# Kernel optimization log

Measured on AMD Instinct MI355X. Metric: run time of the kernel, lower is better.

Reference implementation:

```python
import jax, jax.numpy as jnp
import numpy as np

D = 1024      # d_model
B = 8         # batch
S = 512       # seq
L = 2         # GRU layers
DEPTH = 3     # min_depth == max_depth -> fixed recursion depth
EPS_RMS = 1.1920929e-07  # torch fp32 finfo eps (nn.RMSNorm default)


def setup_inputs() -> dict:
    key = jax.random.key(0)
    ks = jax.random.split(key, 16)

    def glorot(k, shape):
        fan_out, fan_in = shape
        lim = float(np.sqrt(6.0 / (fan_in + fan_out)))
        return jax.random.uniform(k, shape, jnp.float32, -lim, lim)

    gs = float(1.0 / np.sqrt(D))  # torch GRU init: U(-1/sqrt(H), 1/sqrt(H))
    inp = {
        "x": jax.random.normal(ks[0], (B, S, D), jnp.float32),
        # reflect: Linear -> RMSNorm -> GELU -> Linear -> RMSNorm
        "w1": glorot(ks[1], (D, D)), "b1": jnp.zeros(D, jnp.float32),
        "rms1_w": jnp.ones(D, jnp.float32),
        "w2": glorot(ks[2], (D, D)), "b2": jnp.zeros(D, jnp.float32),
        "rms2_w": jnp.ones(D, jnp.float32),
        "residual_weight": jnp.float32(0.5),
        # IntegrationMeasure projections (xavier_uniform, zero bias)
        "whole_w": glorot(ks[3], (D // 2, D)), "whole_b": jnp.zeros(D // 2, jnp.float32),
        "parts_w": glorot(ks[4], (D // 2, D)), "parts_b": jnp.zeros(D // 2, jnp.float32),
        "phi_scale": jnp.float32(1.0), "phi_bias": jnp.float32(0.0),
    }
    ki = 5
    for l in range(L):
        inp[f"wih{l}"] = jax.random.uniform(ks[ki + 0], (3 * D, D), jnp.float32, -gs, gs)
        inp[f"whh{l}"] = jax.random.uniform(ks[ki + 1], (3 * D, D), jnp.float32, -gs, gs)
        inp[f"bih{l}"] = jax.random.uniform(ks[ki + 2], (3 * D,), jnp.float32, -gs, gs)
        inp[f"bhh{l}"] = jax.random.uniform(ks[ki + 3], (3 * D,), jnp.float32, -gs, gs)
        ki += 4
    return inp


def _rmsnorm(x, w):
    ms = jnp.mean(x * x, axis=-1, keepdims=True)
    return x * jax.lax.rsqrt(ms + EPS_RMS) * w


def _gru_layer(seq, h0, Wih, Whh, bih, bhh):
    """seq: [S,B,D], h0: [B,D] -> (outputs [S,B,D], h_final [B,D]). torch gate order r,z,n."""
    def step(h, xt):
        gi = xt @ Wih.T + bih                       # [B, 3D]
        gh = h @ Whh.T + bhh                        # [B, 3D]
        ir, iz, ig = jnp.split(gi, 3, axis=-1)
        hr, hz, hg = jnp.split(gh, 3, axis=-1)
        r = jax.nn.sigmoid(ir + hr)
        z = jax.nn.sigmoid(iz + hz)
        n = jnp.tanh(ig + r * hg)
        hn = (1.0 - z) * n + z * h
        return hn, hn
    hT, ys = jax.lax.scan(step, h0, seq)
    return ys, hT


def reference(x, w1, b1, rms1_w, w2, b2, rms2_w, residual_weight,
              wih0, whh0, bih0, bhh0, wih1, whh1, bih1, bhh1,
              whole_w, whole_b, parts_w, parts_b, phi_scale, phi_bias):
    gru = [(wih0, whh0, bih0, bhh0), (wih1, whh1, bih1, bhh1)]
    batch = x.shape[0]
    hidden = [jnp.zeros((batch, D), x.dtype) for _ in range(L)]
    history = []  # detached states
    phi = None

    for loop in range(DEPTH):
        # self-reflection block
        h = _rmsnorm(x @ w1.T + b1, rms1_w)
        h = jax.nn.gelu(h, approximate=False)
        h = _rmsnorm(h @ w2.T + b2, rms2_w)
        x_ref = x + residual_weight * (h - x)
        # GRU integration (seq-first)
        seq = jnp.transpose(x_ref, (1, 0, 2))       # [S,B,D]
        new_hidden = []
        for l in range(L):
            seq, hT = _gru_layer(seq, hidden[l], *gru[l])
            new_hidden.append(hT)
        hidden = new_hidden
        x = jnp.transpose(seq, (0, 1, 2)).transpose(1, 0, 2)  # [B,S,D]
        # Phi (IntegrationMeasure) -- manifold_norm == L2 norm, fully vectorized
        whole = x @ whole_w.T + whole_b             # [B,S,D/2]
        whole_info = jnp.linalg.norm(whole, axis=-1).mean(axis=-1)  # [B]
        if len(history) == 0:
            phi = jnp.broadcast_to(jax.nn.sigmoid(phi_bias) * 0.3, (batch,))
        else:
            parts = jnp.stack(history) @ parts_w.T + parts_b      # [H,B,S,D/2]
            parts_info = jnp.linalg.norm(parts, axis=-1).mean(axis=-1).mean(axis=0)  # [B]
            raw_phi = (whole_info - parts_info) / (whole_info + 1e-08)
            phi = jnp.clip(phi_scale * raw_phi + phi_bias, 0.0, 1.0)
        history.append(jax.lax.stop_gradient(x))    # torch: x.clone().detach()

    return x, phi
```

## Files before the change

### kernel.cpp

```cpp
#include <hip/hip_runtime.h>
#include <math.h>

#define Dm 1024
#define Bm 8
#define Sm 512

typedef short s16x8 __attribute__((ext_vector_type(8)));
typedef float f32x4 __attribute__((ext_vector_type(4)));
typedef unsigned short u16;
typedef unsigned long long u64;

__device__ __forceinline__ float bf2f(u16 u) {
  union { float f; unsigned v; } x; x.v = (unsigned)u << 16; return x.f;
}
__device__ __forceinline__ u16 f2bf(float f) {
  union { float f; unsigned v; } x; x.f = f;
  unsigned r = x.v + 0x7FFFu + ((x.v >> 16) & 1u);
  return (u16)(r >> 16);
}
__device__ __forceinline__ float sigm(float x) { return 1.f / (1.f + expf(-x)); }

__device__ __forceinline__ u64 cld64(const void* p) {
  return __hip_atomic_load((const u64*)p, __ATOMIC_RELAXED, __HIP_MEMORY_SCOPE_AGENT);
}
__device__ __forceinline__ float cldf(const void* p) {
  return __hip_atomic_load((const float*)p, __ATOMIC_RELAXED, __HIP_MEMORY_SCOPE_AGENT);
}
__device__ __forceinline__ void cx64(void* p, u64 v) {
  u64 old = __hip_atomic_exchange((u64*)p, v, __ATOMIC_RELAXED, __HIP_MEMORY_SCOPE_AGENT);
  asm volatile("" :: "v"(old));
}
__device__ __forceinline__ void cst32(void* p, unsigned v) {
  __hip_atomic_store((unsigned*)p, v, __ATOMIC_RELAXED, __HIP_MEMORY_SCOPE_AGENT);
}

__global__ void k_conv(const float* __restrict__ x, const float* __restrict__ w1,
                       const float* __restrict__ w2, const float* __restrict__ ww,
                       const float* __restrict__ pw,
                       u16* __restrict__ Xb, u16* __restrict__ Wc,
                       float* __restrict__ Hf, u16* __restrict__ Hb,
                       float* __restrict__ sums, unsigned* __restrict__ flags,
                       unsigned* __restrict__ poison)
{
  long gid = (long)blockIdx.x * blockDim.x + threadIdx.x;
  const long N0 = 4194304, N1 = 1048576, N2 = 1048576, N3 = 524288, N4 = 524288;
  const long T = N0 + N1 + N2 + N3 + N4;
  for (long p = gid; p < T; p += (long)gridDim.x * blockDim.x) {
    long q = p;
    if (q < N0) { Xb[q] = f2bf(x[q]); continue; }
    q -= N0;
    if (q < N1) { Wc[q] = f2bf(w1[q]); continue; }
    q -= N1;
    if (q < N2) { Wc[N1 + q] = f2bf(w2[q]); continue; }
    q -= N2;
    if (q < N3) { Wc[N1 + N2 + q] = f2bf(ww[q]); continue; }
    q -= N3;
    Wc[N1 + N2 + N3 + q] = f2bf(pw[q]);
  }
  if (gid < 65536) flags[gid] = 0;
  if (gid < 2 * Bm * Dm) Hf[gid] = 0.f;
  if (gid < 262144) Hb[gid] = 0;
  if (gid < 16) sums[gid] = 0.f;
  if (gid == 0) *poison = 0;
}

template<int MODE>
__global__ __launch_bounds__(512)
void k_gemm(const u16* __restrict__ A, const u16* __restrict__ W,
            const float* __restrict__ bias, const float* __restrict__ nw,
            const u16* __restrict__ XresB, const float* __restrict__ rwp,
            u16* __restrict__ out0, float* __restrict__ sumdst, int Ncols)
{
  __shared__ u16 At[16 * 1024];
  __shared__ float rowsq[16];
  const int tid = threadIdx.x;
  const int lane = tid & 63, wv = tid >> 6;
  const int rlo = lane & 15, khi = lane >> 4;
  const int m0 = blockIdx.x * 16;

  {
    int row = tid & 15, c = tid >> 4;
    const char* src = (const char*)(A + (long)(m0 + row) * Dm);
    char* dst = (char*)At + row * 2048;
    int sw = (row & 7) << 4;
#pragma unroll
    for (int i = 0; i < 4; ++i) {
      int bo = c * 64 + i * 16;
      s16x8 v = *(const s16x8*)(src + bo);
      *(s16x8*)(dst + (bo ^ sw)) = v;
    }
  }
  __syncthreads();

  const int j0 = wv * 128;
  const bool act = j0 < Ncols;
  f32x4 zero4 = {0.f, 0.f, 0.f, 0.f};
  f32x4 acc[8];
#pragma unroll
  for (int jt = 0; jt < 8; ++jt) acc[jt] = zero4;

  if (act) {
    const u16* wbase = W + (long)(j0 + rlo) * Dm + khi * 8;
    const char* abase = (const char*)At + rlo * 2048;
    const int asw = (rlo & 7) << 4;
#pragma unroll
    for (int ks = 0; ks < 32; ++ks) {
      s16x8 a = *(const s16x8*)(abase + (((ks * 32 + khi * 8) * 2) ^ asw));
#pragma unroll
      for (int jt = 0; jt < 8; ++jt) {
        s16x8 b = *(const s16x8*)(wbase + (long)jt * 16 * Dm + ks * 32);
        acc[jt] = __builtin_amdgcn_mfma_f32_16x16x32_bf16(a, b, acc[jt], 0, 0, 0);
      }
    }
  }

  if (tid < 16) rowsq[tid] = 0.f;
  __syncthreads();

  float vals[8][4];
  if (act) {
    float rs[4] = {0.f, 0.f, 0.f, 0.f};
#pragma unroll
    for (int jt = 0; jt < 8; ++jt) {
      float bj = bias[j0 + jt * 16 + rlo];
#pragma unroll
      for (int r = 0; r < 4; ++r) {
        float v = acc[jt][r] + bj;
        vals[jt][r] = v;
        rs[r] += v * v;
      }
    }
#pragma unroll
    for (int r = 0; r < 4; ++r) {
#pragma unroll
      for (int m = 1; m < 16; m <<= 1) rs[r] += __shfl_xor(rs[r], m, 64);
    }
    if (rlo == 0) {
#pragma unroll
      for (int r = 0; r < 4; ++r) atomicAdd(&rowsq[khi * 4 + r], rs[r]);
    }
  }
  __syncthreads();

  if constexpr (MODE == 2) {
    if (tid < 16) {
      int token = m0 + tid;
      atomicAdd(&sumdst[token >> 9], sqrtf(rowsq[tid]));
    }
    return;
  } else {
    float rw = 0.f;
    if constexpr (MODE == 1) rw = rwp[0];
    if (act) {
#pragma unroll
      for (int jt = 0; jt < 8; ++jt) {
        int col = j0 + jt * 16 + rlo;
        float nwv = nw[col];
#pragma unroll
        for (int r = 0; r < 4; ++r) {
          int row = khi * 4 + r;
          int token = m0 + row;
          float ms = rowsq[row] * (1.f / 1024.f) + 1.1920929e-07f;
          float y = vals[jt][r] * rsqrtf(ms) * nwv;
          if constexpr (MODE == 0) {
            y = 0.5f * y * (1.f + erff(y * 0.7071067811865476f));
            out0[(long)token * Dm + col] = f2bf(y);
          } else {
            float xf = bf2f(XresB[(long)token * Dm + col]);
            float xr = xf + rw * (y - xf);
            u16 hi = f2bf(xr);
            float lo = xr - bf2f(hi);
            int s = token & (Sm - 1), b = token >> 9;
            long base = ((long)s * 16 + b) * Dm + col;
            out0[base] = hi;
            out0[base + 8 * Dm] = f2bf(lo);
          }
        }
      }
    }
  }
}

#define SPIN_CAP 2000000

__device__ __forceinline__ bool spin2(const unsigned* pA, bool enA, const unsigned* pB,
                                      unsigned val, unsigned* poison) {
  int spins = 0;
  while (true) {
    bool c = !enA || (__hip_atomic_load(pA, __ATOMIC_RELAXED, __HIP_MEMORY_SCOPE_AGENT) >= val);
    if (pB) c = c && (__hip_atomic_load(pB, __ATOMIC_RELAXED, __HIP_MEMORY_SCOPE_AGENT) >= val);
    if (__all(c)) return true;
    __builtin_amdgcn_s_sleep(1);
    if ((++spins & 255) == 0) {
      if (__hip_atomic_load(poison, __ATOMIC_RELAXED, __HIP_MEMORY_SCOPE_AGENT)) return false;
      if (spins > SPIN_CAP) {
        __hip_atomic_store(poison, 1u, __ATOMIC_RELAXED, __HIP_MEMORY_SCOPE_AGENT);
        return false;
      }
    }
  }
}

__global__ __launch_bounds__(256, 1)
void k_rec(const float* __restrict__ wih0, const float* __restrict__ whh0,
           const float* __restrict__ bih0, const float* __restrict__ bhh0,
           const float* __restrict__ wih1, const float* __restrict__ whh1,
           const float* __restrict__ bih1, const float* __restrict__ bhh1,
           const u16* __restrict__ XrefB,
           float* __restrict__ gi0r, float* __restrict__ gi1r,
           u16* __restrict__ Hb, float* __restrict__ Hf,
           u16* __restrict__ Xb, float* __restrict__ outx,
           unsigned* __restrict__ flags, unsigned* __restrict__ poison, int loop)
{
  __shared__ float part[4][3][16][33];
  __shared__ unsigned pflag;

  const int wg = blockIdx.x;
  const int role = wg >> 5;
  const int w = wg & 31;
  const int d0 = w * 32;
  const int tid = threadIdx.x;
  const int lane = tid & 63, q = tid >> 6;
  const int rlo = lane & 15, khi = lane >> 4;
  const unsigned val = (unsigned)loop + 1u;

  unsigned* F0 = flags;
  unsigned* F1 = flags + 16384;
  unsigned* F2 = flags + 32768;
  unsigned* F3 = flags + 49152;
  u16* Hb0 = Hb;
  u16* Hb1 = Hb + 8 * 16384;

  if (tid == 0) pflag = 0;

  const float* Wsel = (role == 0) ? wih0 : (role == 1) ? whh0 : (role == 2) ? wih1 : whh1;

  s16x8 bfr[8][3][2];
#pragma unroll
  for (int ks = 0; ks < 8; ++ks)
#pragma unroll
    for (int g = 0; g < 3; ++g)
#pragma unroll
      for (int jt = 0; jt < 2; ++jt) {
        int rowj = g * 1024 + d0 + jt * 16 + rlo;
        const float* p = Wsel + (long)rowj * Dm + q * 256 + ks * 32 + khi * 8;
        s16x8 f;
#pragma unroll
        for (int e = 0; e < 8; ++e) f[e] = (short)f2bf(p[e]);
        bfr[ks][g][jt] = f;
      }

  const int ob = tid >> 5, odd = tid & 31, od = d0 + odd;
  float bias_r[3];
  {
    const float* bsel = (role == 0) ? bih0 : (role == 1) ? bhh0 : (role == 2) ? bih1 : bhh1;
#pragma unroll
    for (int g = 0; g < 3; ++g) bias_r[g] = bsel[g * 1024 + od];
  }
  const int layer = (role == 1) ? 0 : 1;
  float hreg = 0.f;
  if (role == 1 || role == 3) hreg = Hf[layer * 8192 + ob * 1024 + od];
  __syncthreads();

  for (int t = 0; t < Sm; ++t) {
    if (q == 0) {
      const unsigned* pA;
      const unsigned* pB = nullptr;
      bool enA;
      bool need = true;
      if (role == 0) {
        pA = &F1[((t >= 8) ? (t - 8) : 0) * 32 + w];
        enA = true;
        need = (t >= 8);
      } else if (role == 1) {
        pA = (lane < 32) ? &F1[((t >= 1) ? (t - 1) : 0) * 32 + lane]
                         : &F2[((t >= 8) ? (t - 8) : 0) * 32 + (lane - 32)];
        enA = (lane < 32) ? (t >= 1) : (t >= 8);
        pB = &F0[t * 32 + w];
      } else if (role == 2) {
        pA = (lane < 32) ? &F1[t * 32 + lane]
                         : &F3[((t >= 8) ? (t - 8) : 0) * 32 + (lane - 32)];
        enA = (lane < 32) ? true : (t >= 8);
      } else {
        pA = &F3[((t >= 1) ? (t - 1) : 0) * 32 + ((lane < 32) ? lane : (lane - 32))];
        enA = (lane < 32) && (t >= 1);
        pB = &F2[t * 32 + w];
      }
      if (need) {
        if (!spin2(pA, enA, pB, val, poison)) { if (lane == 0) pflag = 1; }
      }
    }
    __builtin_amdgcn_sched_barrier(0);
    __syncthreads();
    if (pflag) return;

    float giv[3] = {0.f, 0.f, 0.f};
    if (role == 1 || role == 3) {
      const float* ring = ((role == 1) ? gi0r : gi1r) + ((long)(t & 7) * Bm + ob) * 3072 + od;
      giv[0] = cldf(ring);
      giv[1] = cldf(ring + 1024);
      giv[2] = cldf(ring + 2048);
    }

    s16x8 areg[8];
    if (role == 0) {
      const u16* src = XrefB + (long)t * 16 * Dm + rlo * 1024 + q * 256 + khi * 8;
#pragma unroll
      for (int ks = 0; ks < 8; ++ks)
        areg[ks] = *(const s16x8*)(src + ks * 32);
    } else {
      const u16* base = (role == 1) ? Hb0 + ((t - 1) & 7) * 16384
                      : (role == 2) ? Hb0 + (t & 7) * 16384
                                    : Hb1 + ((t - 1) & 7) * 16384;
      const u16* src = base + rlo * 1024 + q * 256 + khi * 8;
#pragma unroll
      for (int ks = 0; ks < 8; ++ks) {
        union { u64 u[2]; s16x8 v; } tmp;
        tmp.u[0] = cld64(src + ks * 32);
        tmp.u[1] = cld64(src + ks * 32 + 4);
        areg[ks] = tmp.v;
      }
    }

    f32x4 zero4 = {0.f, 0.f, 0.f, 0.f};
    f32x4 acc[3][2];
#pragma unroll
    for (int g = 0; g < 3; ++g) { acc[g][0] = zero4; acc[g][1] = zero4; }
#pragma unroll
    for (int ks = 0; ks < 8; ++ks)
#pragma unroll
      for (int g = 0; g < 3; ++g)
#pragma unroll
        for (int jt = 0; jt < 2; ++jt)
          acc[g][jt] = __builtin_amdgcn_mfma_f32_16x16x32_bf16(areg[ks], bfr[ks][g][jt], acc[g][jt], 0, 0, 0);

#pragma unroll
    for (int g = 0; g < 3; ++g)
#pragma unroll
      for (int jt = 0; jt < 2; ++jt)
#pragma unroll
        for (int r = 0; r < 4; ++r)
          part[q][g][khi * 4 + r][jt * 16 + rlo] = acc[g][jt][r];
    __syncthreads();

    {
      int b = ob, dd = odd;
      float v[3];
#pragma unroll
      for (int g = 0; g < 3; ++g) {
        float sv = 0.f;
#pragma unroll
        for (int qq = 0; qq < 4; ++qq)
          sv += part[qq][g][b][dd] + part[qq][g][8 + b][dd];
        v[g] = sv;
      }
      if (role == 0 || role == 2) {
        float* ring = ((role == 0) ? gi0r : gi1r) + ((long)(t & 7) * Bm + b) * 3072 + od;
#pragma unroll
        for (int g = 0; g < 3; ++g) {
          float fg = v[g] + bias_r[g];
          float pg = __shfl_xor(fg, 1, 64);
          if ((dd & 1) == 0) {
            union { float f; unsigned u; } a0, a1;
            a0.f = fg; a1.f = pg;
            u64 pk = (u64)a0.u | ((u64)a1.u << 32);
            cx64(ring + g * 1024, pk);
          }
        }
      } else {
        float gr = giv[0] + v[0] + bias_r[0];
        float gz = giv[1] + v[1] + bias_r[1];
        float ghn = v[2] + bias_r[2];
        float rr = sigm(gr), zz = sigm(gz);
        float nn = tanhf(giv[2] + rr * ghn);
        float hn = (1.f - zz) * nn + zz * hreg;
        hreg = hn;
        u16 hi = f2bf(hn);
        u16 lo = f2bf(hn - bf2f(hi));
        unsigned myv = (unsigned)hi | ((unsigned)lo << 16);
        unsigned p1 = __shfl_xor(myv, 1, 64);
        unsigned hiPair = (myv & 0xFFFFu) | ((p1 & 0xFFFFu) << 16);
        unsigned loPair = (myv >> 16) | (p1 & 0xFFFF0000u);
        unsigned hp2 = __shfl_xor(hiPair, 2, 64);
        unsigned lp2 = __shfl_xor(loPair, 2, 64);
        if ((dd & 3) == 0) {
          u64 hq = (u64)hiPair | ((u64)hp2 << 32);
          u64 lq = (u64)loPair | ((u64)lp2 << 32);
          u16* hb = ((role == 1) ? Hb0 : Hb1) + (t & 7) * 16384;
          cx64(hb + b * 1024 + od, hq);
          cx64(hb + 8192 + b * 1024 + od, lq);
        }
        if (role == 3) {
          long xi = ((long)b * Sm + t) * Dm + od;
          Xb[xi] = hi;
          if (outx) outx[xi] = hn;
        }
        if (t == Sm - 1) Hf[layer * 8192 + b * 1024 + od] = hreg;
      }
    }
    __syncthreads();
    __builtin_amdgcn_sched_barrier(0);
    if (tid == 0) {
      unsigned* F = (role == 0) ? F0 : (role == 1) ? F1 : (role == 2) ? F2 : F3;
      cst32(&F[t * 32 + w], val);
    }
  }
}

__global__ void k_phi(const float* __restrict__ sums, const float* __restrict__ psc,
                      const float* __restrict__ pbi, float* __restrict__ out)
{
  int b = threadIdx.x;
  if (b < 8) {
    float whole = sums[8 + b] * (1.f / 512.f);
    float parts = sums[b] * (1.f / 1024.f);
    float raw = (whole - parts) / (whole + 1e-8f);
    float phi = psc[0] * raw + pbi[0];
    phi = fminf(fmaxf(phi, 0.f), 1.f);
    out[(long)Bm * Sm * Dm + b] = phi;
  }
}

extern "C" void kernel_launch(void* const* d_in, const int* in_sizes, int n_in,
                              void* d_out, int out_size, void* d_ws, size_t ws_size,
                              hipStream_t stream)
{
  (void)in_sizes; (void)n_in; (void)out_size;
  const float* b1   = (const float*)d_in[2];
  const float* r1w  = (const float*)d_in[3];
  const float* b2   = (const float*)d_in[5];
  const float* r2w  = (const float*)d_in[6];
  const float* rw   = (const float*)d_in[7];
  const float* wb   = (const float*)d_in[9];
  const float* pb   = (const float*)d_in[11];
  const float* psc  = (const float*)d_in[12];
  const float* pbi  = (const float*)d_in[13];
  const float* wih0 = (const float*)d_in[14];
  const float* whh0 = (const float*)d_in[15];
  const float* bih0 = (const float*)d_in[16];
  const float* bhh0 = (const float*)d_in[17];
  const float* wih1 = (const float*)d_in[18];
  const float* whh1 = (const float*)d_in[19];
  const float* bih1 = (const float*)d_in[20];
  const float* bhh1 = (const float*)d_in[21];
  float* out = (float*)d_out;

  if (ws_size < 45000000) return;

  char* ws = (char*)d_ws;
  size_t off = 0;
  auto alloc = [&](size_t bytes) -> char* {
    char* p = ws + off;
    off += (bytes + 255) & ~(size_t)255;
    return p;
  };
  u16*      Xb    = (u16*)  alloc((size_t)4194304 * 2);
  u16*      T1    = (u16*)  alloc((size_t)4194304 * 2);
  u16*      XrefB = (u16*)  alloc((size_t)2 * 4194304 * 2);
  float*    gi0r  = (float*)alloc((size_t)8 * 8 * 3072 * 4);
  float*    gi1r  = (float*)alloc((size_t)8 * 8 * 3072 * 4);
  u16*      Hb    = (u16*)  alloc((size_t)2 * 8 * 16384 * 2);
  float*    Hf    = (float*)alloc((size_t)2 * 8192 * 4);
  u16*      Wc    = (u16*)  alloc((size_t)3145728 * 2);
  float*    sums  = (float*)alloc(16 * 4);
  unsigned* flags = (unsigned*)alloc((size_t)65536 * 4);
  unsigned* poi   = (unsigned*)alloc(256);

  u16* WcW1 = Wc;
  u16* WcW2 = Wc + 1048576;
  u16* WcWW = Wc + 2097152;
  u16* WcPW = Wc + 2621440;

  k_conv<<<2048, 256, 0, stream>>>((const float*)d_in[0], (const float*)d_in[1],
                                   (const float*)d_in[4], (const float*)d_in[8],
                                   (const float*)d_in[10],
                                   Xb, Wc, Hf, Hb, sums, flags, poi);

  for (int loop = 0; loop < 3; ++loop) {
    k_gemm<0><<<256, 512, 0, stream>>>(Xb, WcW1, b1, r1w, nullptr, nullptr, T1, nullptr, 1024);
    k_gemm<1><<<256, 512, 0, stream>>>(T1, WcW2, b2, r2w, Xb, rw, XrefB, nullptr, 1024);
    k_rec<<<128, 256, 0, stream>>>(wih0, whh0, bih0, bhh0, wih1, whh1, bih1, bhh1,
                                   XrefB, gi0r, gi1r, Hb, Hf, Xb,
                                   (loop == 2) ? out : nullptr, flags, poi, loop);
    if (loop < 2)
      k_gemm<2><<<256, 512, 0, stream>>>(Xb, WcPW, pb, nullptr, nullptr, nullptr, nullptr, sums, 512);
    else
      k_gemm<2><<<256, 512, 0, stream>>>(Xb, WcWW, wb, nullptr, nullptr, nullptr, nullptr, sums + 8, 512);
  }
  k_phi<<<1, 64, 0, stream>>>(sums, psc, pbi, out);
}
```

Measured before the change: 10.67 ms.

## Repartition GRU recurrence over 64 workgroups of 512 threads with 64-column slices

The persistent recurrent kernel now runs 64 workgroups of 512 threads instead of 128 of 256. Each workgroup owns 64 hidden columns, and its 8 waves split K in 128-wide chunks, with a two-phase shared-memory reduction. This halves the number of per-step flags each workgroup must poll and the number of workgroups in the cross-workgroup dependency chain, which is meant to cut synchronisation latency per timestep. In exchange each workgroup does twice the MFMA work per step, uses more shared memory, and adds an extra __syncthreads round per step.

```diff
diff --git a/kernel.cpp b/kernel.cpp
--- a/kernel.cpp
+++ b/kernel.cpp
@@ -57,7 +57,7 @@
     q -= N3;
     Wc[N1 + N2 + N3 + q] = f2bf(pw[q]);
   }
-  if (gid < 65536) flags[gid] = 0;
+  if (gid < 32768) flags[gid] = 0;
   if (gid < 2 * Bm * Dm) Hf[gid] = 0.f;
   if (gid < 262144) Hb[gid] = 0;
   if (gid < 16) sums[gid] = 0.f;
@@ -201,7 +201,7 @@
   }
 }
 
-__global__ __launch_bounds__(256, 1)
+__global__ __launch_bounds__(512, 2)
 void k_rec(const float* __restrict__ wih0, const float* __restrict__ whh0,
            const float* __restrict__ bih0, const float* __restrict__ bhh0,
            const float* __restrict__ wih1, const float* __restrict__ whh1,
@@ -212,22 +212,22 @@
            u16* __restrict__ Xb, float* __restrict__ outx,
            unsigned* __restrict__ flags, unsigned* __restrict__ poison, int loop)
 {
-  __shared__ float part[4][3][16][33];
+  __shared__ float part[4][3][16][65];
   __shared__ unsigned pflag;
 
   const int wg = blockIdx.x;
-  const int role = wg >> 5;
-  const int w = wg & 31;
-  const int d0 = w * 32;
+  const int role = wg >> 4;
+  const int w = wg & 15;
+  const int d0 = w * 64;
   const int tid = threadIdx.x;
   const int lane = tid & 63, q = tid >> 6;
   const int rlo = lane & 15, khi = lane >> 4;
   const unsigned val = (unsigned)loop + 1u;
 
   unsigned* F0 = flags;
-  unsigned* F1 = flags + 16384;
-  unsigned* F2 = flags + 32768;
-  unsigned* F3 = flags + 49152;
+  unsigned* F1 = flags + 8192;
+  unsigned* F2 = flags + 16384;
+  unsigned* F3 = flags + 24576;
   u16* Hb0 = Hb;
   u16* Hb1 = Hb + 8 * 16384;
 
@@ -235,22 +235,22 @@
 
   const float* Wsel = (role == 0) ? wih0 : (role == 1) ? whh0 : (role == 2) ? wih1 : whh1;
 
-  s16x8 bfr[8][3][2];
-#pragma unroll
-  for (int ks = 0; ks < 8; ++ks)
+  s16x8 bfr[4][3][4];
+#pragma unroll
+  for (int ks = 0; ks < 4; ++ks)
 #pragma unroll
     for (int g = 0; g < 3; ++g)
 #pragma unroll
-      for (int jt = 0; jt < 2; ++jt) {
+      for (int jt = 0; jt < 4; ++jt) {
         int rowj = g * 1024 + d0 + jt * 16 + rlo;
-        const float* p = Wsel + (long)rowj * Dm + q * 256 + ks * 32 + khi * 8;
+        const float* p = Wsel + (long)rowj * Dm + q * 128 + ks * 32 + khi * 8;
         s16x8 f;
 #pragma unroll
         for (int e = 0; e < 8; ++e) f[e] = (short)f2bf(p[e]);
         bfr[ks][g][jt] = f;
       }
 
-  const int ob = tid >> 5, odd = tid & 31, od = d0 + odd;
+  const int ob = q, odd = lane, od = d0 + odd;
   float bias_r[3];
   {
     const float* bsel = (role == 0) ? bih0 : (role == 1) ? bhh0 : (role == 2) ? bih1 : bhh1;
@@ -264,27 +264,28 @@
 
   for (int t = 0; t < Sm; ++t) {
     if (q == 0) {
+      bool need = true;
       const unsigned* pA;
       const unsigned* pB = nullptr;
       bool enA;
-      bool need = true;
       if (role == 0) {
-        pA = &F1[((t >= 8) ? (t - 8) : 0) * 32 + w];
-        enA = true;
+        pA = &F1[((t >= 8) ? (t - 8) : 0) * 16 + w];
+        enA = (lane == 0);
         need = (t >= 8);
       } else if (role == 1) {
-        pA = (lane < 32) ? &F1[((t >= 1) ? (t - 1) : 0) * 32 + lane]
-                         : &F2[((t >= 8) ? (t - 8) : 0) * 32 + (lane - 32)];
-        enA = (lane < 32) ? (t >= 1) : (t >= 8);
-        pB = &F0[t * 32 + w];
+        pA = (lane < 16) ? &F1[((t >= 1) ? (t - 1) : 0) * 16 + lane]
+           : (lane < 32) ? &F2[((t >= 8) ? (t - 8) : 0) * 16 + (lane - 16)]
+                         : &F0[t * 16 + w];
+        enA = (lane < 16) ? (t >= 1) : (lane < 32) ? (t >= 8) : false;
+        pB = &F0[t * 16 + w];
       } else if (role == 2) {
-        pA = (lane < 32) ? &F1[t * 32 + lane]
-                         : &F3[((t >= 8) ? (t - 8) : 0) * 32 + (lane - 32)];
-        enA = (lane < 32) ? true : (t >= 8);
+        pA = &F1[t * 16 + ((lane < 16) ? lane : 0)];
+        enA = (lane < 16);
+        pB = (t >= 8) ? &F3[(t - 8) * 16 + w] : nullptr;
       } else {
-        pA = &F3[((t >= 1) ? (t - 1) : 0) * 32 + ((lane < 32) ? lane : (lane - 32))];
-        enA = (lane < 32) && (t >= 1);
-        pB = &F2[t * 32 + w];
+        pA = &F3[((t >= 1) ? (t - 1) : 0) * 16 + ((lane < 16) ? lane : 0)];
+        enA = (lane < 16) && (t >= 1);
+        pB = &F2[t * 16 + w];
       }
       if (need) {
         if (!spin2(pA, enA, pB, val, poison)) { if (lane == 0) pflag = 1; }
@@ -302,19 +303,19 @@
       giv[2] = cldf(ring + 2048);
     }
 
-    s16x8 areg[8];
+    s16x8 areg[4];
     if (role == 0) {
-      const u16* src = XrefB + (long)t * 16 * Dm + rlo * 1024 + q * 256 + khi * 8;
-#pragma unroll
-      for (int ks = 0; ks < 8; ++ks)
+      const u16* src = XrefB + (long)t * 16 * Dm + rlo * 1024 + q * 128 + khi * 8;
+#pragma unroll
+      for (int ks = 0; ks < 4; ++ks)
         areg[ks] = *(const s16x8*)(src + ks * 32);
     } else {
       const u16* base = (role == 1) ? Hb0 + ((t - 1) & 7) * 16384
                       : (role == 2) ? Hb0 + (t & 7) * 16384
                                     : Hb1 + ((t - 1) & 7) * 16384;
-      const u16* src = base + rlo * 1024 + q * 256 + khi * 8;
-#pragma unroll
-      for (int ks = 0; ks < 8; ++ks) {
+      const u16* src = base + rlo * 1024 + q * 128 + khi * 8;
+#pragma unroll
+      for (int ks = 0; ks < 4; ++ks) {
         union { u64 u[2]; s16x8 v; } tmp;
         tmp.u[0] = cld64(src + ks * 32);
         tmp.u[1] = cld64(src + ks * 32 + 4);
@@ -323,25 +324,40 @@
     }
 
     f32x4 zero4 = {0.f, 0.f, 0.f, 0.f};
-    f32x4 acc[3][2];
-#pragma unroll
-    for (int g = 0; g < 3; ++g) { acc[g][0] = zero4; acc[g][1] = zero4; }
-#pragma unroll
-    for (int ks = 0; ks < 8; ++ks)
-#pragma unroll
-      for (int g = 0; g < 3; ++g)
-#pragma unroll
-        for (int jt = 0; jt < 2; ++jt)
-          acc[g][jt] = __builtin_amdgcn_mfma_f32_16x16x32_bf16(areg[ks], bfr[ks][g][jt], acc[g][jt], 0, 0, 0);
-
-#pragma unroll
-    for (int g = 0; g < 3; ++g)
-#pragma unroll
-      for (int jt = 0; jt < 2; ++jt)
-#pragma unroll
-        for (int r = 0; r < 4; ++r)
-          part[q][g][khi * 4 + r][jt * 16 + rlo] = acc[g][jt][r];
-    __syncthreads();
+#pragma unroll
+    for (int jg = 0; jg < 2; ++jg) {
+      f32x4 acc[3][2];
+#pragma unroll
+      for (int g = 0; g < 3; ++g) { acc[g][0] = zero4; acc[g][1] = zero4; }
+#pragma unroll
+      for (int ks = 0; ks < 4; ++ks)
+#pragma unroll
+        for (int g = 0; g < 3; ++g)
+#pragma unroll
+          for (int j2 = 0; j2 < 2; ++j2)
+            acc[g][j2] = __builtin_amdgcn_mfma_f32_16x16x32_bf16(
+                areg[ks], bfr[ks][g][jg * 2 + j2], acc[g][j2], 0, 0, 0);
+      if (q < 4) {
+#pragma unroll
+        for (int g = 0; g < 3; ++g)
+#pragma unroll
+          for (int j2 = 0; j2 < 2; ++j2)
+#pragma unroll
+            for (int r = 0; r < 4; ++r)
+              part[q][g][khi * 4 + r][jg * 32 + j2 * 16 + rlo] = acc[g][j2][r];
+      }
+      __syncthreads();
+      if (q >= 4) {
+#pragma unroll
+        for (int g = 0; g < 3; ++g)
+#pragma unroll
+          for (int j2 = 0; j2 < 2; ++j2)
+#pragma unroll
+            for (int r = 0; r < 4; ++r)
+              part[q - 4][g][khi * 4 + r][jg * 32 + j2 * 16 + rlo] += acc[g][j2][r];
+      }
+      __syncthreads();
+    }
 
     {
       int b = ob, dd = odd;
@@ -350,8 +366,8 @@
       for (int g = 0; g < 3; ++g) {
         float sv = 0.f;
 #pragma unroll
-        for (int qq = 0; qq < 4; ++qq)
-          sv += part[qq][g][b][dd] + part[qq][g][8 + b][dd];
+        for (int p = 0; p < 4; ++p)
+          sv += part[p][g][b][dd] + part[p][g][8 + b][dd];
         v[g] = sv;
       }
       if (role == 0 || role == 2) {
@@ -402,7 +418,7 @@
     __builtin_amdgcn_sched_barrier(0);
     if (tid == 0) {
       unsigned* F = (role == 0) ? F0 : (role == 1) ? F1 : (role == 2) ? F2 : F3;
-      cst32(&F[t * 32 + w], val);
+      cst32(&F[t * 16 + w], val);
     }
   }
 }
@@ -463,7 +479,7 @@
   float*    Hf    = (float*)alloc((size_t)2 * 8192 * 4);
   u16*      Wc    = (u16*)  alloc((size_t)3145728 * 2);
   float*    sums  = (float*)alloc(16 * 4);
-  unsigned* flags = (unsigned*)alloc((size_t)65536 * 4);
+  unsigned* flags = (unsigned*)alloc((size_t)32768 * 4);
   unsigned* poi   = (unsigned*)alloc(256);
 
   u16* WcW1 = Wc;
@@ -479,9 +495,9 @@
   for (int loop = 0; loop < 3; ++loop) {
     k_gemm<0><<<256, 512, 0, stream>>>(Xb, WcW1, b1, r1w, nullptr, nullptr, T1, nullptr, 1024);
     k_gemm<1><<<256, 512, 0, stream>>>(T1, WcW2, b2, r2w, Xb, rw, XrefB, nullptr, 1024);
-    k_rec<<<128, 256, 0, stream>>>(wih0, whh0, bih0, bhh0, wih1, whh1, bih1, bhh1,
-                                   XrefB, gi0r, gi1r, Hb, Hf, Xb,
-                                   (loop == 2) ? out : nullptr, flags, poi, loop);
+    k_rec<<<64, 512, 0, stream>>>(wih0, whh0, bih0, bhh0, wih1, whh1, bih1, bhh1,
+                                  XrefB, gi0r, gi1r, Hb, Hf, Xb,
+                                  (loop == 2) ? out : nullptr, flags, poi, loop);
     if (loop < 2)
       k_gemm<2><<<256, 512, 0, stream>>>(Xb, WcPW, pb, nullptr, nullptr, nullptr, nullptr, sums, 512);
     else
```

Result: slower. 13.20 ms (+23.7%).
